# Kernel optimization log

Measured on AMD Instinct MI355X. Metric: run time of the kernel, lower is better.

Reference implementation:

```python
import jax, jax.numpy as jnp
import numpy as np


def gcn_conv(x, src, dst, norm, W, b, n_nodes):
    # PyG GCNConv: out[dst] = sum_edges norm * (x @ W)[src] + b
    h = x @ W                      # [N, F_out]
    msg = h[src] * norm[:, None]   # [E', F_out] gather + scale
    out = jax.ops.segment_sum(msg, dst, num_segments=n_nodes)
    return out + b


def _gcn_norm(edge_index, n_nodes):
    # add self loops, compute symmetric normalization deg^-1/2[src]*deg^-1/2[dst]
    loop = jnp.arange(n_nodes, dtype=edge_index.dtype)
    src = jnp.concatenate([edge_index[0], loop])
    dst = jnp.concatenate([edge_index[1], loop])
    deg = jnp.zeros((n_nodes,), jnp.float32).at[dst].add(1.0)
    dinv = jnp.where(deg > 0, jax.lax.rsqrt(deg), 0.0)
    norm = dinv[src] * dinv[dst]
    return src, dst, norm


def setup_inputs() -> dict:
    key = jax.random.key(0)
    ks = jax.random.split(key, 5)
    N, E, C_in, C_out = 50000, 800000, 128, 32
    H = 2 * C_out
    x = jax.random.normal(ks[0], (N, C_in), jnp.float32)
    edge_index = jax.random.randint(ks[1], (2, E), 0, N, jnp.int64)
    s1 = 1.0 / np.sqrt(C_in)
    s2 = 1.0 / np.sqrt(H)
    W1 = jax.random.uniform(ks[2], (C_in, H), jnp.float32, -s1, s1)
    b1 = jnp.zeros((H,), jnp.float32)
    W_mu = jax.random.uniform(ks[3], (H, C_out), jnp.float32, -s2, s2)
    b_mu = jnp.zeros((C_out,), jnp.float32)
    W_ls = jax.random.uniform(ks[4], (H, C_out), jnp.float32, -s2, s2)
    b_ls = jnp.zeros((C_out,), jnp.float32)
    return {"x": x, "edge_index": edge_index, "W1": W1, "b1": b1,
            "W_mu": W_mu, "b_mu": b_mu, "W_ls": W_ls, "b_ls": b_ls}


def reference(x, edge_index, W1, b1, W_mu, b_mu, W_ls, b_ls):
    n_nodes = x.shape[0]
    src, dst, norm = _gcn_norm(edge_index, n_nodes)
    h = jax.nn.relu(gcn_conv(x, src, dst, norm, W1, b1, n_nodes))
    mu = gcn_conv(h, src, dst, norm, W_mu, b_mu, n_nodes)
    logstd = gcn_conv(h, src, dst, norm, W_ls, b_ls, n_nodes)
    return mu, logstd
```

## Files before the change

kernel.cpp:

```cpp
#include <hip/hip_runtime.h>
#include <hip/hip_fp16.h>
#include <math.h>


typedef unsigned int uint;
typedef unsigned short ushort;
typedef __attribute__((ext_vector_type(8))) short short8;
typedef __attribute__((ext_vector_type(4))) float f32x4;

#define CAPB 5120

__device__ __forceinline__ ushort f2bf(float x) {
    uint u = __float_as_uint(x);
    u += 0x7fffu + ((u >> 16) & 1u);
    return (ushort)(u >> 16);
}
__device__ __forceinline__ float bf2f(ushort h) {
    return __uint_as_float((uint)h << 16);
}

__global__ __launch_bounds__(256) void k_scatter(
        const int* __restrict__ src, const int* __restrict__ dst,
        int* __restrict__ bcount, uint* __restrict__ recs, int E) {
    __shared__ int h[256];
    __shared__ int rb[256];
    const int tid = threadIdx.x;
    h[tid] = 0;
    __syncthreads();
    const int base = blockIdx.x * 2048;
    uint rec[8]; int rk[8];
    #pragma unroll
    for (int k = 0; k < 8; ++k) {
        int i = base + k * 256 + tid;
        if (i < E) {
            int s = __builtin_nontemporal_load(src + i);
            int d = __builtin_nontemporal_load(dst + i);
            int b = d >> 8;
            rec[k] = (uint)s | ((uint)(d & 255) << 16) | ((uint)b << 24);
            rk[k] = atomicAdd(&h[b], 1);
        }
    }
    __syncthreads();
    const int hv = h[tid];
    rb[tid] = hv ? atomicAdd(&bcount[tid], hv) : 0;
    __syncthreads();
    #pragma unroll
    for (int k = 0; k < 8; ++k) {
        int i = base + k * 256 + tid;
        if (i < E) {
            int b = rec[k] >> 24;
            int pos = rb[b] + rk[k];
            if (pos < CAPB) recs[(size_t)b * CAPB + pos] = rec[k];
        }
    }
}

__global__ __launch_bounds__(256, 2) void k_phaseBG(
        const uint* __restrict__ recs, const int* __restrict__ bcount,
        const float* __restrict__ x, const float* __restrict__ W1,
        int* __restrict__ row_ptr, float* __restrict__ dinv,
        ushort* __restrict__ edges, ushort* __restrict__ hp,
        int N, int E, int NBUCK) {
    __shared__ int h[256];
    __shared__ int p[256];
    __shared__ float sdinv[256];
    __shared__ __align__(16) char ubuf[32768];
    uint* rstage = (uint*)ubuf;
    const int tid = threadIdx.x;
    const int bx  = blockIdx.x;
    int v = min(bcount[tid], CAPB);
    p[tid] = v;
    h[tid] = 0;
    __syncthreads();
    #pragma unroll
    for (int off = 1; off < 256; off <<= 1) {
        int xv = (tid >= off) ? p[tid - off] : 0;
        __syncthreads();
        p[tid] += xv;
        __syncthreads();
    }
    const int cnt = min(bcount[bx], CAPB);
    const int bs  = p[bx] - cnt;
    for (int i = tid; i < cnt; i += 256) {
        uint r = recs[(size_t)bx * CAPB + i];
        rstage[i] = r;
        atomicAdd(&h[(r >> 16) & 255], 1);
    }
    __syncthreads();
    v = h[tid];
    p[tid] = v;
    __syncthreads();
    #pragma unroll
    for (int off = 1; off < 256; off <<= 1) {
        int xv = (tid >= off) ? p[tid - off] : 0;
        __syncthreads();
        p[tid] += xv;
        __syncthreads();
    }
    const int excl = p[tid] - v;
    const int node = bx * 256 + tid;
    const float dvt = rsqrtf((float)(v + 1));
    sdinv[tid] = dvt;
    if (node < N) {
        row_ptr[node] = bs + excl;
        dinv[node] = dvt;
    }
    if (bx == NBUCK - 1 && tid == 0) row_ptr[N] = E;
    h[tid] = excl;
    __syncthreads();
    for (int i = tid; i < cnt; i += 256) {
        uint r = rstage[i];
        int pos = atomicAdd(&h[(r >> 16) & 255], 1);
        edges[bs + pos] = (ushort)(r & 0xffffu);
    }
    __syncthreads();
    ushort (*Wt)[136] = (ushort(*)[136])ubuf;
    #pragma unroll
    for (int it = 0; it < 8; ++it) {
        int idx = (it * 256 + tid) * 4;
        int k = idx >> 6, c = idx & 63;
        float4 wv = *(const float4*)(W1 + idx);
        Wt[c + 0][k] = f2bf(wv.x);
        Wt[c + 1][k] = f2bf(wv.y);
        Wt[c + 2][k] = f2bf(wv.z);
        Wt[c + 3][k] = f2bf(wv.w);
    }
    __syncthreads();
    const int w = tid >> 6, l = tid & 63;
    const int m = l & 15, q = l >> 4;
    #pragma unroll 1
    for (int t = 0; t < 4; ++t) {
        const int lrow0 = t * 64 + w * 16;
        const int row0  = bx * 256 + lrow0;
        const size_t arow = (size_t)min(row0 + m, N - 1);
        f32x4 acc0 = {0.f, 0.f, 0.f, 0.f}, acc1 = acc0, acc2 = acc0, acc3 = acc0;
        #pragma unroll
        for (int kc = 0; kc < 4; ++kc) {
            const int kofs = kc * 32 + q * 8;
            const float4* xr = (const float4*)(x + arow * 128 + kofs);
            float4 xa = xr[0], xb = xr[1];
            short8 a;
            a[0] = (short)f2bf(xa.x); a[1] = (short)f2bf(xa.y);
            a[2] = (short)f2bf(xa.z); a[3] = (short)f2bf(xa.w);
            a[4] = (short)f2bf(xb.x); a[5] = (short)f2bf(xb.y);
            a[6] = (short)f2bf(xb.z); a[7] = (short)f2bf(xb.w);
            short8 b0 = *(const short8*)&Wt[m][kofs];
            short8 b1 = *(const short8*)&Wt[m + 16][kofs];
            short8 b2 = *(const short8*)&Wt[m + 32][kofs];
            short8 b3 = *(const short8*)&Wt[m + 48][kofs];
            acc0 = __builtin_amdgcn_mfma_f32_16x16x32_bf16(a, b0, acc0, 0, 0, 0);
            acc1 = __builtin_amdgcn_mfma_f32_16x16x32_bf16(a, b1, acc1, 0, 0, 0);
            acc2 = __builtin_amdgcn_mfma_f32_16x16x32_bf16(a, b2, acc2, 0, 0, 0);
            acc3 = __builtin_amdgcn_mfma_f32_16x16x32_bf16(a, b3, acc3, 0, 0, 0);
        }
        #pragma unroll
        for (int r = 0; r < 4; ++r) {
            int lrow = lrow0 + q * 4 + r;
            int row  = bx * 256 + lrow;
            if (row >= N) continue;
            float dv = sdinv[lrow];
            ushort* hr = hp + (size_t)row * 64 + m;
            hr[0]  = f2bf(acc0[r] * dv);
            hr[16] = f2bf(acc1[r] * dv);
            hr[32] = f2bf(acc2[r] * dv);
            hr[48] = f2bf(acc3[r] * dv);
        }
    }
}

__device__ __forceinline__ void gather_grp8(
        const uint* __restrict__ hp, const ushort* __restrict__ edges,
        int beg, int end, int E, int sl, float4& a0, float4& a1) {
    for (int base = beg; base < end; base += 8) {
        const int mrec = (int)edges[min(base + sl, E - 1)];
        const int cnt = end - base;
        if (cnt >= 8) {
            #pragma unroll
            for (int i = 0; i < 8; ++i) {
                const int r = __shfl(mrec, i, 8);
                const uint4 v = *(const uint4*)(hp + (size_t)r * 32 + 4 * sl);
                a0.x += __uint_as_float(v.x << 16);
                a0.y += __uint_as_float(v.x & 0xffff0000u);
                a0.z += __uint_as_float(v.y << 16);
                a0.w += __uint_as_float(v.y & 0xffff0000u);
                a1.x += __uint_as_float(v.z << 16);
                a1.y += __uint_as_float(v.z & 0xffff0000u);
                a1.z += __uint_as_float(v.w << 16);
                a1.w += __uint_as_float(v.w & 0xffff0000u);
            }
        } else {
            #pragma unroll
            for (int i = 0; i < 7; ++i) {
                const int r = __shfl(mrec, min(i, cnt - 1), 8);
                uint4 v = *(const uint4*)(hp + (size_t)r * 32 + 4 * sl);
                if (i >= cnt) { v.x = 0u; v.y = 0u; v.z = 0u; v.w = 0u; }
                a0.x += __uint_as_float(v.x << 16);
                a0.y += __uint_as_float(v.x & 0xffff0000u);
                a0.z += __uint_as_float(v.y << 16);
                a0.w += __uint_as_float(v.y & 0xffff0000u);
                a1.x += __uint_as_float(v.z << 16);
                a1.y += __uint_as_float(v.z & 0xffff0000u);
                a1.z += __uint_as_float(v.w << 16);
                a1.w += __uint_as_float(v.w & 0xffff0000u);
            }
        }
    }
}

__global__ __launch_bounds__(256, 6) void k_gather1(
        const uint* __restrict__ hp, const int* __restrict__ row_ptr,
        const ushort* __restrict__ edges, const float* __restrict__ dinv,
        const float* __restrict__ b1, uint* __restrict__ ho, int N, int E) {
    const int lane = threadIdx.x & 63;
    const int sl = lane & 7;
    const int n = blockIdx.x * 32 + ((threadIdx.x >> 6) << 3) + (lane >> 3);
    const int nc = min(n, N - 1);
    const int beg = row_ptr[nc], end = row_ptr[nc + 1];
    float4 a0 = {0.f, 0.f, 0.f, 0.f}, a1 = a0;
    gather_grp8(hp, edges, beg, end, E, sl, a0, a1);
    const float dv = dinv[nc];
    const uint4 sv = *(const uint4*)(hp + (size_t)nc * 32 + 4 * sl);
    const float4 bA = ((const float4*)b1)[2 * sl];
    const float4 bB = ((const float4*)b1)[2 * sl + 1];
    float s0 = a0.x + bf2f((ushort)sv.x);
    float s1 = a0.y + bf2f((ushort)(sv.x >> 16));
    float s2 = a0.z + bf2f((ushort)sv.y);
    float s3 = a0.w + bf2f((ushort)(sv.y >> 16));
    float s4 = a1.x + bf2f((ushort)sv.z);
    float s5 = a1.y + bf2f((ushort)(sv.z >> 16));
    float s6 = a1.z + bf2f((ushort)sv.w);
    float s7 = a1.w + bf2f((ushort)(sv.w >> 16));
    float h0 = fmaxf(fmaf(dv, s0, bA.x), 0.f) * dv;
    float h1 = fmaxf(fmaf(dv, s1, bA.y), 0.f) * dv;
    float h2 = fmaxf(fmaf(dv, s2, bA.z), 0.f) * dv;
    float h3 = fmaxf(fmaf(dv, s3, bA.w), 0.f) * dv;
    float h4 = fmaxf(fmaf(dv, s4, bB.x), 0.f) * dv;
    float h5 = fmaxf(fmaf(dv, s5, bB.y), 0.f) * dv;
    float h6 = fmaxf(fmaf(dv, s6, bB.z), 0.f) * dv;
    float h7 = fmaxf(fmaf(dv, s7, bB.w), 0.f) * dv;
    if (n < N) {
        uint4 o;
        o.x = (uint)f2bf(h0) | ((uint)f2bf(h1) << 16);
        o.y = (uint)f2bf(h2) | ((uint)f2bf(h3) << 16);
        o.z = (uint)f2bf(h4) | ((uint)f2bf(h5) << 16);
        o.w = (uint)f2bf(h6) | ((uint)f2bf(h7) << 16);
        *(uint4*)(ho + (size_t)n * 32 + 4 * sl) = o;
    }
}

__global__ __launch_bounds__(256, 6) void k_gather2(
        const uint* __restrict__ hp, const int* __restrict__ row_ptr,
        const ushort* __restrict__ edges, const float* __restrict__ dinv,
        const float* __restrict__ Wmu, const float* __restrict__ Wls,
        const float* __restrict__ bmu, const float* __restrict__ bls,
        float* __restrict__ out, int N, int E) {
    __shared__ __align__(16) float hs[4][8][64];
    const int lane = threadIdx.x & 63;
    const int sl = lane & 7, grp = lane >> 3;
    const int w = threadIdx.x >> 6;
    const int n = blockIdx.x * 32 + (w << 3) + grp;
    const int nc = min(n, N - 1);
    const int beg = row_ptr[nc], end = row_ptr[nc + 1];
    float4 a0 = {0.f, 0.f, 0.f, 0.f}, a1 = a0;
    gather_grp8(hp, edges, beg, end, E, sl, a0, a1);
    const float dv = dinv[nc];
    const uint4 sv = *(const uint4*)(hp + (size_t)nc * 32 + 4 * sl);
    float4 gA, gB;
    gA.x = dv * (a0.x + bf2f((ushort)sv.x));
    gA.y = dv * (a0.y + bf2f((ushort)(sv.x >> 16)));
    gA.z = dv * (a0.z + bf2f((ushort)sv.y));
    gA.w = dv * (a0.w + bf2f((ushort)(sv.y >> 16)));
    gB.x = dv * (a1.x + bf2f((ushort)sv.z));
    gB.y = dv * (a1.y + bf2f((ushort)(sv.z >> 16)));
    gB.z = dv * (a1.z + bf2f((ushort)sv.w));
    gB.w = dv * (a1.w + bf2f((ushort)(sv.w >> 16)));
    *(float4*)&hs[w][grp][8 * sl]     = gA;
    *(float4*)&hs[w][grp][8 * sl + 4] = gB;
    const float* Wsel = (lane < 32) ? (Wmu + lane) : (Wls + (lane - 32));
    const float bias  = (lane < 32) ? bmu[lane] : bls[lane - 32];
    #pragma unroll
    for (int p = 0; p < 2; ++p) {
        float c0 = 0.f, c1 = 0.f, c2 = 0.f, c3 = 0.f;
        #pragma unroll 4
        for (int k = 0; k < 64; ++k) {
            float wv = Wsel[k * 32];
            c0 = fmaf(hs[w][p * 4 + 0][k], wv, c0);
            c1 = fmaf(hs[w][p * 4 + 1][k], wv, c1);
            c2 = fmaf(hs[w][p * 4 + 2][k], wv, c2);
            c3 = fmaf(hs[w][p * 4 + 3][k], wv, c3);
        }
        const int n0 = blockIdx.x * 32 + (w << 3) + p * 4;
        float cs[4] = {c0, c1, c2, c3};
        #pragma unroll
        for (int gg = 0; gg < 4; ++gg) {
            int nn = n0 + gg;
            if (nn >= N) break;
            float t = cs[gg] + bias;
            if (lane < 32) out[(size_t)nn * 32 + lane] = t;
            else           out[(size_t)N * 32 + (size_t)nn * 32 + (lane - 32)] = t;
        }
    }
}

extern "C" void kernel_launch(void* const* d_in, const int* in_sizes, int n_in,
                              void* d_out, int out_size, void* d_ws, size_t ws_size,
                              hipStream_t stream) {
    const float* x   = (const float*)d_in[0];
    const int*   ei  = (const int*)d_in[1];
    const float* W1  = (const float*)d_in[2];
    const float* b1  = (const float*)d_in[3];
    const float* Wmu = (const float*)d_in[4];
    const float* bmu = (const float*)d_in[5];
    const float* Wls = (const float*)d_in[6];
    const float* bls = (const float*)d_in[7];
    float* out = (float*)d_out;

    const int N = in_sizes[0] / 128;
    const int E = in_sizes[1] / 2;
    const int* src = ei;
    const int* dst = ei + E;
    const int SB    = (E + 2047) / 2048;
    const int NBUCK = (N + 255) / 256;
    const int NG    = (N + 31) / 32;

    char* w = (char*)d_ws;
    auto carve = [&](size_t bytes) { char* p = w; w += (bytes + 1023) & ~(size_t)1023; return p; };
    int*    bcount  = (int*)   carve(256 * 4);
    uint*   recs    = (uint*)  carve((size_t)NBUCK * CAPB * 4);
    int*    row_ptr = (int*)   carve((size_t)(N + 1) * 4);
    float*  dinv    = (float*) carve((size_t)N * 4);
    ushort* edges   = (ushort*)carve((size_t)E * 2);
    ushort* h_pre   = (ushort*)carve((size_t)N * 64 * 2);
    ushort* h_mid   = (ushort*)carve((size_t)N * 64 * 2);

    hipMemsetAsync(bcount, 0, 256 * 4, stream);
    k_scatter <<<SB, 256, 0, stream>>>(src, dst, bcount, recs, E);
    k_phaseBG <<<NBUCK, 256, 0, stream>>>(recs, bcount, x, W1, row_ptr, dinv,
                                          edges, h_pre, N, E, NBUCK);
    k_gather1 <<<NG, 256, 0, stream>>>((const uint*)h_pre, row_ptr, edges, dinv,
                                       b1, (uint*)h_mid, N, E);
    k_gather2 <<<NG, 256, 0, stream>>>((const uint*)h_mid, row_ptr, edges, dinv,
                                       Wmu, Wls, bmu, bls, out, N, E);
}
```

Measured before the change: 169.6 us.

## Replace global bucket atomics with per-block count matrix and fixed-slot records

The scatter kernel no longer reserves space with global atomics on a per-bucket counter. Each block writes its local histogram to a count matrix and stores its records in a fixed slot per (bucket, block) pair, capped at 48 entries. The phase kernel sums that count matrix column to get bucket totals and prefix sums, then compacts the slots through a shared-memory cursor. This drops the global atomic contention and the memset, but adds SB reads of the count matrix per thread, a serial per-slot copy loop, and possible silent truncation if a slot overflows.

Result: slower. 213.3 us (+25.8%).

```diff
diff --git a/kernel.cpp b/kernel.cpp
--- a/kernel.cpp
+++ b/kernel.cpp
@@ -8,7 +8,7 @@
 typedef __attribute__((ext_vector_type(8))) short short8;
 typedef __attribute__((ext_vector_type(4))) float f32x4;
 
-#define CAPB 5120
+#define CAPC 48
 
 __device__ __forceinline__ ushort f2bf(float x) {
     uint u = __float_as_uint(x);
@@ -21,13 +21,13 @@
 
 __global__ __launch_bounds__(256) void k_scatter(
         const int* __restrict__ src, const int* __restrict__ dst,
-        int* __restrict__ bcount, uint* __restrict__ recs, int E) {
+        int* __restrict__ cmat, uint* __restrict__ recs, int E, int SB) {
     __shared__ int h[256];
-    __shared__ int rb[256];
     const int tid = threadIdx.x;
+    const int bx  = blockIdx.x;
     h[tid] = 0;
     __syncthreads();
-    const int base = blockIdx.x * 2048;
+    const int base = bx * 2048;
     uint rec[8]; int rk[8];
     #pragma unroll
     for (int k = 0; k < 8; ++k) {
@@ -41,36 +41,38 @@
         }
     }
     __syncthreads();
-    const int hv = h[tid];
-    rb[tid] = hv ? atomicAdd(&bcount[tid], hv) : 0;
-    __syncthreads();
+    cmat[bx * 256 + tid] = h[tid];
     #pragma unroll
     for (int k = 0; k < 8; ++k) {
         int i = base + k * 256 + tid;
         if (i < E) {
             int b = rec[k] >> 24;
-            int pos = rb[b] + rk[k];
-            if (pos < CAPB) recs[(size_t)b * CAPB + pos] = rec[k];
+            if (rk[k] < CAPC)
+                recs[((size_t)b * SB + bx) * CAPC + rk[k]] = rec[k];
         }
     }
 }
 
 __global__ __launch_bounds__(256, 2) void k_phaseBG(
-        const uint* __restrict__ recs, const int* __restrict__ bcount,
+        const uint* __restrict__ recs, const int* __restrict__ cmat,
         const float* __restrict__ x, const float* __restrict__ W1,
         int* __restrict__ row_ptr, float* __restrict__ dinv,
         ushort* __restrict__ edges, ushort* __restrict__ hp,
-        int N, int E, int NBUCK) {
+        int N, int E, int NBUCK, int SB) {
     __shared__ int h[256];
     __shared__ int p[256];
     __shared__ float sdinv[256];
+    __shared__ int curs;
     __shared__ __align__(16) char ubuf[32768];
     uint* rstage = (uint*)ubuf;
     const int tid = threadIdx.x;
     const int bx  = blockIdx.x;
-    int v = min(bcount[tid], CAPB);
-    p[tid] = v;
+    int tot = 0;
+    for (int sb = 0; sb < SB; ++sb)
+        tot += min(cmat[sb * 256 + tid], CAPC);
+    p[tid] = tot;
     h[tid] = 0;
+    if (tid == 0) curs = 0;
     __syncthreads();
     #pragma unroll
     for (int off = 1; off < 256; off <<= 1) {
@@ -79,15 +81,23 @@
         p[tid] += xv;
         __syncthreads();
     }
-    const int cnt = min(bcount[bx], CAPB);
-    const int bs  = p[bx] - cnt;
-    for (int i = tid; i < cnt; i += 256) {
-        uint r = recs[(size_t)bx * CAPB + i];
-        rstage[i] = r;
-        atomicAdd(&h[(r >> 16) & 255], 1);
-    }
-    __syncthreads();
-    v = h[tid];
+    const int pincl = p[bx];
+    const int cnt   = pincl - (bx ? p[bx - 1] : 0);
+    const int bs    = pincl - cnt;
+    for (int sb = tid; sb < SB; sb += 256) {
+        int c = min(cmat[sb * 256 + bx], CAPC);
+        if (c) {
+            int o = atomicAdd(&curs, c);
+            const uint* rp = recs + ((size_t)bx * SB + sb) * CAPC;
+            for (int i = 0; i < c; ++i) {
+                uint r = rp[i];
+                rstage[o + i] = r;
+                atomicAdd(&h[(r >> 16) & 255], 1);
+            }
+        }
+    }
+    __syncthreads();
+    int v = h[tid];
     p[tid] = v;
     __syncthreads();
     #pragma unroll
@@ -325,18 +335,17 @@
 
     char* w = (char*)d_ws;
     auto carve = [&](size_t bytes) { char* p = w; w += (bytes + 1023) & ~(size_t)1023; return p; };
-    int*    bcount  = (int*)   carve(256 * 4);
-    uint*   recs    = (uint*)  carve((size_t)NBUCK * CAPB * 4);
+    int*    cmat    = (int*)   carve((size_t)SB * 256 * 4);
+    uint*   recs    = (uint*)  carve((size_t)NBUCK * SB * CAPC * 4);
     int*    row_ptr = (int*)   carve((size_t)(N + 1) * 4);
     float*  dinv    = (float*) carve((size_t)N * 4);
     ushort* edges   = (ushort*)carve((size_t)E * 2);
     ushort* h_pre   = (ushort*)carve((size_t)N * 64 * 2);
     ushort* h_mid   = (ushort*)carve((size_t)N * 64 * 2);
 
-    hipMemsetAsync(bcount, 0, 256 * 4, stream);
-    k_scatter <<<SB, 256, 0, stream>>>(src, dst, bcount, recs, E);
-    k_phaseBG <<<NBUCK, 256, 0, stream>>>(recs, bcount, x, W1, row_ptr, dinv,
-                                          edges, h_pre, N, E, NBUCK);
+    k_scatter <<<SB, 256, 0, stream>>>(src, dst, cmat, recs, E, SB);
+    k_phaseBG <<<NBUCK, 256, 0, stream>>>(recs, cmat, x, W1, row_ptr, dinv,
+                                          edges, h_pre, N, E, NBUCK, SB);
     k_gather1 <<<NG, 256, 0, stream>>>((const uint*)h_pre, row_ptr, edges, dinv,
                                        b1, (uint*)h_mid, N, E);
     k_gather2 <<<NG, 256, 0, stream>>>((const uint*)h_mid, row_ptr, edges, dinv,
```

## Fuse edge bucketing into build kernel by having each block scan all dst

Applied to the files above, without the earlier changes.

Drops the separate scatter kernel, the bucket counter memset and the intermediate record buffer. Each bucket block now scans the whole dst array, keeps the edges whose destination falls in its 256-node range, and reads src indirectly for them. Each bucket gets a fixed-capacity segment of the edge array, and a per-bucket 257-entry row pointer table replaces the global CSR prefix. This saves one launch and the record round-trip, but every block must re-read the full dst array and pays per-edge shared atomics, which multiplies read traffic by the bucket count.

Result: slower. 421.3 us (+148.4%).

```diff
diff --git a/kernel.cpp b/kernel.cpp
--- a/kernel.cpp
+++ b/kernel.cpp
@@ -19,58 +19,40 @@
     return __uint_as_float((uint)h << 16);
 }
 
-__global__ __launch_bounds__(256) void k_scatter(
+__global__ __launch_bounds__(256, 2) void k_buildg(
         const int* __restrict__ src, const int* __restrict__ dst,
-        int* __restrict__ bcount, uint* __restrict__ recs, int E) {
-    __shared__ int h[256];
-    __shared__ int rb[256];
-    const int tid = threadIdx.x;
-    h[tid] = 0;
-    __syncthreads();
-    const int base = blockIdx.x * 2048;
-    uint rec[8]; int rk[8];
-    #pragma unroll
-    for (int k = 0; k < 8; ++k) {
-        int i = base + k * 256 + tid;
-        if (i < E) {
-            int s = __builtin_nontemporal_load(src + i);
-            int d = __builtin_nontemporal_load(dst + i);
-            int b = d >> 8;
-            rec[k] = (uint)s | ((uint)(d & 255) << 16) | ((uint)b << 24);
-            rk[k] = atomicAdd(&h[b], 1);
-        }
-    }
-    __syncthreads();
-    const int hv = h[tid];
-    rb[tid] = hv ? atomicAdd(&bcount[tid], hv) : 0;
-    __syncthreads();
-    #pragma unroll
-    for (int k = 0; k < 8; ++k) {
-        int i = base + k * 256 + tid;
-        if (i < E) {
-            int b = rec[k] >> 24;
-            int pos = rb[b] + rk[k];
-            if (pos < CAPB) recs[(size_t)b * CAPB + pos] = rec[k];
-        }
-    }
-}
-
-__global__ __launch_bounds__(256, 2) void k_phaseBG(
-        const uint* __restrict__ recs, const int* __restrict__ bcount,
         const float* __restrict__ x, const float* __restrict__ W1,
-        int* __restrict__ row_ptr, float* __restrict__ dinv,
+        int* __restrict__ rp2, float* __restrict__ dinv,
         ushort* __restrict__ edges, ushort* __restrict__ hp,
         int N, int E, int NBUCK) {
     __shared__ int h[256];
     __shared__ int p[256];
     __shared__ float sdinv[256];
-    __shared__ __align__(16) char ubuf[32768];
-    uint* rstage = (uint*)ubuf;
+    __shared__ int cnt;
+    __shared__ __align__(16) char ubuf[20480];
+    uint* marr = (uint*)ubuf;
     const int tid = threadIdx.x;
     const int bx  = blockIdx.x;
-    int v = min(bcount[tid], CAPB);
+    h[tid] = 0;
+    if (tid == 0) cnt = 0;
+    __syncthreads();
+    const int E4 = E >> 2;
+    for (int i4 = tid; i4 < E4; i4 += 256) {
+        const int4 d4 = ((const int4*)dst)[i4];
+        const int i0 = i4 * 4;
+        int d;
+        d = d4.x; if ((d >> 8) == bx) { int ix = atomicAdd(&cnt, 1); atomicAdd(&h[d & 255], 1); if (ix < CAPB) marr[ix] = (uint)(i0    ) | ((uint)(d & 255) << 24); }
+        d = d4.y; if ((d >> 8) == bx) { int ix = atomicAdd(&cnt, 1); atomicAdd(&h[d & 255], 1); if (ix < CAPB) marr[ix] = (uint)(i0 + 1) | ((uint)(d & 255) << 24); }
+        d = d4.z; if ((d >> 8) == bx) { int ix = atomicAdd(&cnt, 1); atomicAdd(&h[d & 255], 1); if (ix < CAPB) marr[ix] = (uint)(i0 + 2) | ((uint)(d & 255) << 24); }
+        d = d4.w; if ((d >> 8) == bx) { int ix = atomicAdd(&cnt, 1); atomicAdd(&h[d & 255], 1); if (ix < CAPB) marr[ix] = (uint)(i0 + 3) | ((uint)(d & 255) << 24); }
+    }
+    for (int i = E4 * 4 + tid; i < E; i += 256) {
+        int d = dst[i];
+        if ((d >> 8) == bx) { int ix = atomicAdd(&cnt, 1); atomicAdd(&h[d & 255], 1); if (ix < CAPB) marr[ix] = (uint)i | ((uint)(d & 255) << 24); }
+    }
+    __syncthreads();
+    int v = h[tid];
     p[tid] = v;
-    h[tid] = 0;
     __syncthreads();
     #pragma unroll
     for (int off = 1; off < 256; off <<= 1) {
@@ -79,51 +61,33 @@
         p[tid] += xv;
         __syncthreads();
     }
-    const int cnt = min(bcount[bx], CAPB);
-    const int bs  = p[bx] - cnt;
-    for (int i = tid; i < cnt; i += 256) {
-        uint r = recs[(size_t)bx * CAPB + i];
-        rstage[i] = r;
-        atomicAdd(&h[(r >> 16) & 255], 1);
-    }
-    __syncthreads();
-    v = h[tid];
-    p[tid] = v;
-    __syncthreads();
-    #pragma unroll
-    for (int off = 1; off < 256; off <<= 1) {
-        int xv = (tid >= off) ? p[tid - off] : 0;
-        __syncthreads();
-        p[tid] += xv;
-        __syncthreads();
-    }
     const int excl = p[tid] - v;
     const int node = bx * 256 + tid;
     const float dvt = rsqrtf((float)(v + 1));
     sdinv[tid] = dvt;
-    if (node < N) {
-        row_ptr[node] = bs + excl;
-        dinv[node] = dvt;
-    }
-    if (bx == NBUCK - 1 && tid == 0) row_ptr[N] = E;
+    rp2[bx * 257 + tid] = bx * CAPB + excl;
+    if (tid == 255) rp2[bx * 257 + 256] = bx * CAPB + excl + v;
+    if (node < N) dinv[node] = dvt;
     h[tid] = excl;
     __syncthreads();
-    for (int i = tid; i < cnt; i += 256) {
-        uint r = rstage[i];
-        int pos = atomicAdd(&h[(r >> 16) & 255], 1);
-        edges[bs + pos] = (ushort)(r & 0xffffu);
+    const int c = min(cnt, CAPB);
+    for (int j = tid; j < c; j += 256) {
+        const uint r = marr[j];
+        const int s = src[r & 0xffffff];
+        const int pos = atomicAdd(&h[r >> 24], 1);
+        if (pos < CAPB) edges[(size_t)bx * CAPB + pos] = (ushort)s;
     }
     __syncthreads();
     ushort (*Wt)[136] = (ushort(*)[136])ubuf;
     #pragma unroll
     for (int it = 0; it < 8; ++it) {
         int idx = (it * 256 + tid) * 4;
-        int k = idx >> 6, c = idx & 63;
+        int k = idx >> 6, ccol = idx & 63;
         float4 wv = *(const float4*)(W1 + idx);
-        Wt[c + 0][k] = f2bf(wv.x);
-        Wt[c + 1][k] = f2bf(wv.y);
-        Wt[c + 2][k] = f2bf(wv.z);
-        Wt[c + 3][k] = f2bf(wv.w);
+        Wt[ccol + 0][k] = f2bf(wv.x);
+        Wt[ccol + 1][k] = f2bf(wv.y);
+        Wt[ccol + 2][k] = f2bf(wv.z);
+        Wt[ccol + 3][k] = f2bf(wv.w);
     }
     __syncthreads();
     const int w = tid >> 6, l = tid & 63;
@@ -170,9 +134,9 @@
 
 __device__ __forceinline__ void gather_grp8(
         const uint* __restrict__ hp, const ushort* __restrict__ edges,
-        int beg, int end, int E, int sl, float4& a0, float4& a1) {
+        int beg, int end, int ECAP, int sl, float4& a0, float4& a1) {
     for (int base = beg; base < end; base += 8) {
-        const int mrec = (int)edges[min(base + sl, E - 1)];
+        const int mrec = (int)edges[min(base + sl, ECAP - 1)];
         const int cnt = end - base;
         if (cnt >= 8) {
             #pragma unroll
@@ -208,16 +172,17 @@
 }
 
 __global__ __launch_bounds__(256, 6) void k_gather1(
-        const uint* __restrict__ hp, const int* __restrict__ row_ptr,
+        const uint* __restrict__ hp, const int* __restrict__ rp2,
         const ushort* __restrict__ edges, const float* __restrict__ dinv,
-        const float* __restrict__ b1, uint* __restrict__ ho, int N, int E) {
+        const float* __restrict__ b1, uint* __restrict__ ho, int N, int ECAP) {
     const int lane = threadIdx.x & 63;
     const int sl = lane & 7;
     const int n = blockIdx.x * 32 + ((threadIdx.x >> 6) << 3) + (lane >> 3);
     const int nc = min(n, N - 1);
-    const int beg = row_ptr[nc], end = row_ptr[nc + 1];
+    const int beg = rp2[(nc >> 8) * 257 + (nc & 255)];
+    const int end = rp2[(nc >> 8) * 257 + (nc & 255) + 1];
     float4 a0 = {0.f, 0.f, 0.f, 0.f}, a1 = a0;
-    gather_grp8(hp, edges, beg, end, E, sl, a0, a1);
+    gather_grp8(hp, edges, beg, end, ECAP, sl, a0, a1);
     const float dv = dinv[nc];
     const uint4 sv = *(const uint4*)(hp + (size_t)nc * 32 + 4 * sl);
     const float4 bA = ((const float4*)b1)[2 * sl];
@@ -249,20 +214,21 @@
 }
 
 __global__ __launch_bounds__(256, 6) void k_gather2(
-        const uint* __restrict__ hp, const int* __restrict__ row_ptr,
+        const uint* __restrict__ hp, const int* __restrict__ rp2,
         const ushort* __restrict__ edges, const float* __restrict__ dinv,
         const float* __restrict__ Wmu, const float* __restrict__ Wls,
         const float* __restrict__ bmu, const float* __restrict__ bls,
-        float* __restrict__ out, int N, int E) {
+        float* __restrict__ out, int N, int ECAP) {
     __shared__ __align__(16) float hs[4][8][64];
     const int lane = threadIdx.x & 63;
     const int sl = lane & 7, grp = lane >> 3;
     const int w = threadIdx.x >> 6;
     const int n = blockIdx.x * 32 + (w << 3) + grp;
     const int nc = min(n, N - 1);
-    const int beg = row_ptr[nc], end = row_ptr[nc + 1];
+    const int beg = rp2[(nc >> 8) * 257 + (nc & 255)];
+    const int end = rp2[(nc >> 8) * 257 + (nc & 255) + 1];
     float4 a0 = {0.f, 0.f, 0.f, 0.f}, a1 = a0;
-    gather_grp8(hp, edges, beg, end, E, sl, a0, a1);
+    gather_grp8(hp, edges, beg, end, ECAP, sl, a0, a1);
     const float dv = dinv[nc];
     const uint4 sv = *(const uint4*)(hp + (size_t)nc * 32 + 4 * sl);
     float4 gA, gB;
@@ -319,26 +285,22 @@
     const int E = in_sizes[1] / 2;
     const int* src = ei;
     const int* dst = ei + E;
-    const int SB    = (E + 2047) / 2048;
     const int NBUCK = (N + 255) / 256;
     const int NG    = (N + 31) / 32;
+    const int ECAP  = NBUCK * CAPB;
 
     char* w = (char*)d_ws;
     auto carve = [&](size_t bytes) { char* p = w; w += (bytes + 1023) & ~(size_t)1023; return p; };
-    int*    bcount  = (int*)   carve(256 * 4);
-    uint*   recs    = (uint*)  carve((size_t)NBUCK * CAPB * 4);
-    int*    row_ptr = (int*)   carve((size_t)(N + 1) * 4);
+    int*    rp2     = (int*)   carve((size_t)NBUCK * 257 * 4);
     float*  dinv    = (float*) carve((size_t)N * 4);
-    ushort* edges   = (ushort*)carve((size_t)E * 2);
+    ushort* edges   = (ushort*)carve((size_t)ECAP * 2);
     ushort* h_pre   = (ushort*)carve((size_t)N * 64 * 2);
     ushort* h_mid   = (ushort*)carve((size_t)N * 64 * 2);
 
-    hipMemsetAsync(bcount, 0, 256 * 4, stream);
-    k_scatter <<<SB, 256, 0, stream>>>(src, dst, bcount, recs, E);
-    k_phaseBG <<<NBUCK, 256, 0, stream>>>(recs, bcount, x, W1, row_ptr, dinv,
+    k_buildg  <<<NBUCK, 256, 0, stream>>>(src, dst, x, W1, rp2, dinv,
                                           edges, h_pre, N, E, NBUCK);
-    k_gather1 <<<NG, 256, 0, stream>>>((const uint*)h_pre, row_ptr, edges, dinv,
-                                       b1, (uint*)h_mid, N, E);
-    k_gather2 <<<NG, 256, 0, stream>>>((const uint*)h_mid, row_ptr, edges, dinv,
-                                       Wmu, Wls, bmu, bls, out, N, E);
-}
+    k_gather1 <<<NG, 256, 0, stream>>>((const uint*)h_pre, rp2, edges, dinv,
+                                       b1, (uint*)h_mid, N, ECAP);
+    k_gather2 <<<NG, 256, 0, stream>>>((const uint*)h_mid, rp2, edges, dinv,
+                                       Wmu, Wls, bmu, bls, out, N, ECAP);
+}
```
